# Kernel tuning notes

Hardware: AMD Instinct MI355X
Metric: run time of the kernel (lower is better)

## Reference

```python
import jax, jax.numpy as jnp
import numpy as np

D_MODEL, D_STATE, EXPAND = 1024, 32, 2
D_INNER = D_MODEL * EXPAND
B, L = 2, 2048


def setup_inputs() -> dict:
    key = jax.random.key(0)
    ks = jax.random.split(key, 10)
    s = 0.02
    return {
        "x": jax.random.normal(ks[0], (B, L, D_MODEL), dtype=jnp.float32),
        "W_in": jax.random.normal(ks[1], (D_INNER * 2, D_MODEL), dtype=jnp.float32) * s,
        "conv_w": jax.random.normal(ks[2], (D_INNER, 1, 3), dtype=jnp.float32) * 0.3,
        "conv_b": jax.random.normal(ks[3], (D_INNER,), dtype=jnp.float32) * 0.01,
        "A_log": jax.random.normal(ks[4], (D_INNER, D_STATE), dtype=jnp.float32),
        "D_skip": jnp.ones((D_INNER,), dtype=jnp.float32),
        "W_xproj": jax.random.normal(ks[5], (D_STATE * 2 + 1, D_INNER), dtype=jnp.float32) * s,
        "W_dt": jax.random.normal(ks[6], (D_INNER, 1), dtype=jnp.float32) * s,
        "b_dt": jax.random.normal(ks[7], (D_INNER,), dtype=jnp.float32) * 0.01,
        "alpha": jnp.asarray(0.5, dtype=jnp.float32),
        "W_out": jax.random.normal(ks[8], (D_MODEL, D_INNER), dtype=jnp.float32) * s,
    }


def _silu(v):
    return v * jax.nn.sigmoid(v)


def _forward(x, W_in, conv_w, conv_b, A_log, D_skip, W_xproj, W_dt, b_dt, alpha, W_out):
    # in_proj: (B, L, 2*d_inner) -> split into x_in, z
    xz = x @ W_in.T
    x_in, z = jnp.split(xz, 2, axis=-1)

    # depthwise conv1d, kernel 3, padding 1 (same-length, non-causal, as in source)
    xc = jax.lax.conv_general_dilated(
        x_in.transpose(0, 2, 1), conv_w, window_strides=(1,), padding=[(1, 1)],
        dimension_numbers=("NCH", "OIH", "NCH"), feature_group_count=D_INNER,
    ) + conv_b[None, :, None]
    x_conv = _silu(xc.transpose(0, 2, 1))  # (B, L, d_inner)

    # x_proj -> dt_raw (1), B_ssm (N), C_ssm (N)
    proj = x_conv @ W_xproj.T
    dt_raw = proj[..., :1]
    B_ssm = proj[..., 1:1 + D_STATE]
    C_ssm = proj[..., 1 + D_STATE:]
    dt = jax.nn.softplus(dt_raw @ W_dt.T + b_dt)  # (B, L, d_inner)

    A_real = -jnp.exp(A_log)           # (d_inner, d_state)
    a = jax.nn.sigmoid(alpha)

    def step(h, inp):
        dt_t, B_t, C_t, u_t = inp      # (B,d_inner), (B,N), (B,N), (B,d_inner)
        dtA = A_real[None] * dt_t[:, :, None]               # (B, d_inner, N)
        A_d = a * jnp.exp(dtA) + (1.0 - a) / (1.0 - 0.5 * dtA + 1e-6)
        h = A_d * h + (dt_t * u_t)[:, :, None] * B_t[:, None, :]
        y_t = jnp.einsum("bn,bdn->bd", C_t, h) + D_skip * u_t
        return h, y_t

    h0 = jnp.zeros((x.shape[0], D_INNER, D_STATE), dtype=x.dtype)
    xs = (dt.transpose(1, 0, 2), B_ssm.transpose(1, 0, 2),
          C_ssm.transpose(1, 0, 2), x_conv.transpose(1, 0, 2))
    _, ys = jax.lax.scan(step, h0, xs)   # (L, B, d_inner)
    y = ys.transpose(1, 0, 2) * _silu(z)
    return y @ W_out.T


def reference(x, W_in, conv_w, conv_b, A_log, D_skip, W_xproj, W_dt, b_dt, alpha, W_out):
    return _forward(x, W_in, conv_w, conv_b, A_log, D_skip, W_xproj, W_dt, b_dt, alpha, W_out)
```

## Files before the change

kernel.cpp:

```cpp
#include <hip/hip_runtime.h>

#define DM   1024
#define DI   2048
#define DST  32
#define NB   2
#define LSEQ 2048
#define BL   (NB*LSEQ)
#define LC   64
#define NC   32

using bf16   = __bf16;
using bf16x4 = __attribute__((ext_vector_type(4))) __bf16;
using bf16x8 = __attribute__((ext_vector_type(8))) __bf16;
using f32x4  = __attribute__((ext_vector_type(4))) float;
using f16x2  = __attribute__((ext_vector_type(2))) _Float16;

static __device__ __forceinline__ float sigmoidf_(float x) {
  return 1.f / (1.f + __expf(-x));
}

static __device__ __forceinline__ f16x2 pack_f16x2(float a, float b) {
  return __builtin_bit_cast(f16x2, __builtin_amdgcn_cvt_pkrtz(a, b));
}

static __device__ __forceinline__ float exp2_(float x) {
#if __has_builtin(__builtin_amdgcn_exp2f)
  return __builtin_amdgcn_exp2f(x);
#else
  return exp2f(x);
#endif
}

__global__ __launch_bounds__(256) void cast_bf16_kernel(
    const float* __restrict__ in, bf16* __restrict__ out, int n4) {
  int i = blockIdx.x * 256 + threadIdx.x;
  if (i >= n4) return;
  f32x4 v = ((const f32x4*)in)[i];
  bf16x4 o;
  #pragma unroll
  for (int j = 0; j < 4; ++j) o[j] = (bf16)v[j];
  ((bf16x4*)out)[i] = o;
}

__global__ __launch_bounds__(256) void padcast_wxp_kernel(
    const float* __restrict__ in, bf16* __restrict__ out) {
  int i = blockIdx.x * 256 + threadIdx.x;
  int k4 = i & 511;
  int r  = i >> 9;
  int src = (r < 64) ? (r + 1) : ((r == 127) ? 0 : -1);
  f32x4 v = {0.f, 0.f, 0.f, 0.f};
  if (src >= 0) v = *(const f32x4*)(in + (size_t)src * 2048 + k4 * 4);
  bf16x4 o;
  #pragma unroll
  for (int j = 0; j < 4; ++j) o[j] = (bf16)v[j];
  ((bf16x4*)out)[i] = o;
}

__global__ __launch_bounds__(256) void gemm_bt(
    const bf16* __restrict__ A, const bf16* __restrict__ B,
    float* __restrict__ C, int M, int N, int K) {
  __shared__ bf16 As[128][40];
  __shared__ bf16 Bs[128][40];

  int tid  = threadIdx.x;
  int bm   = blockIdx.y, bn = blockIdx.x;
  int row0 = bm * 128, col0 = bn * 128;
  int w    = tid >> 6, lane = tid & 63;
  int wr   = w >> 1, wc = w & 1;
  int lr   = lane & 15, lk = lane >> 4;

  f32x4 acc[4][4];
  #pragma unroll
  for (int i = 0; i < 4; ++i)
    #pragma unroll
    for (int j = 0; j < 4; ++j) acc[i][j] = f32x4{0.f, 0.f, 0.f, 0.f};

  int srow = tid >> 1;
  int scol = (tid & 1) * 16;
  const bf16* Ag = A + (size_t)(row0 + srow) * K + scol;
  const bf16* Bg = B + (size_t)(col0 + srow) * K + scol;

  for (int k0 = 0; k0 < K; k0 += 32) {
    *(bf16x8*)&As[srow][scol]     = *(const bf16x8*)(Ag + k0);
    *(bf16x8*)&As[srow][scol + 8] = *(const bf16x8*)(Ag + k0 + 8);
    *(bf16x8*)&Bs[srow][scol]     = *(const bf16x8*)(Bg + k0);
    *(bf16x8*)&Bs[srow][scol + 8] = *(const bf16x8*)(Bg + k0 + 8);
    __syncthreads();

    bf16x8 af[4], bff[4];
    #pragma unroll
    for (int mi = 0; mi < 4; ++mi)
      af[mi] = *(const bf16x8*)&As[wr * 64 + mi * 16 + lr][lk * 8];
    #pragma unroll
    for (int ni = 0; ni < 4; ++ni)
      bff[ni] = *(const bf16x8*)&Bs[wc * 64 + ni * 16 + lr][lk * 8];

    #pragma unroll
    for (int mi = 0; mi < 4; ++mi)
      #pragma unroll
      for (int ni = 0; ni < 4; ++ni)
        acc[mi][ni] = __builtin_amdgcn_mfma_f32_16x16x32_bf16(
            af[mi], bff[ni], acc[mi][ni], 0, 0, 0);
    __syncthreads();
  }

  #pragma unroll
  for (int mi = 0; mi < 4; ++mi)
    #pragma unroll
    for (int ni = 0; ni < 4; ++ni) {
      int r0 = row0 + wr * 64 + mi * 16 + lk * 4;
      int c  = col0 + wc * 64 + ni * 16 + lr;
      #pragma unroll
      for (int r = 0; r < 4; ++r)
        C[(size_t)(r0 + r) * N + c] = acc[mi][ni][r];
    }
}

__global__ __launch_bounds__(256) void conv_silu_kernel(
    const float* __restrict__ xz, bf16* __restrict__ xconv,
    const float* __restrict__ conv_w, const float* __restrict__ conv_b) {
  int i = blockIdx.x * 256 + threadIdx.x;
  int d4 = i & 511;
  int d  = d4 * 4;
  int bl = i >> 9;
  int l  = bl & (LSEQ - 1);

  const float* base = xz + (size_t)bl * (2 * DI) + d;
  f32x4 zero = {0.f, 0.f, 0.f, 0.f};
  f32x4 xm = (l > 0)        ? *(const f32x4*)(base - 2 * DI) : zero;
  f32x4 xc = *(const f32x4*)(base);
  f32x4 xp = (l < LSEQ - 1) ? *(const f32x4*)(base + 2 * DI) : zero;

  bf16x4 o;
  #pragma unroll
  for (int j = 0; j < 4; ++j) {
    float w0 = conv_w[(d + j) * 3 + 0];
    float w1 = conv_w[(d + j) * 3 + 1];
    float w2 = conv_w[(d + j) * 3 + 2];
    float v = fmaf(w0, xm[j], fmaf(w1, xc[j], fmaf(w2, xp[j], conv_b[d + j])));
    v = v * sigmoidf_(v);
    o[j] = (bf16)v;
  }
  *(bf16x4*)(xconv + (size_t)bl * DI + d) = o;
}

__global__ __launch_bounds__(256) void dtprep_kernel(
    const float* __restrict__ proj, const bf16* __restrict__ xconv,
    const float* __restrict__ W_dt, const float* __restrict__ b_dt,
    unsigned int* __restrict__ dtp) {
  int i = blockIdx.x * 256 + threadIdx.x;
  int d4 = (i & 511) * 4;
  int bl = i >> 9;
  float dtraw = proj[(size_t)bl * 128 + 127];
  f32x4 wd = *(const f32x4*)(W_dt + d4);
  f32x4 bd = *(const f32x4*)(b_dt + d4);
  bf16x4 uu = *(const bf16x4*)(xconv + (size_t)bl * DI + d4);
  uint4 o;
  #pragma unroll
  for (int j = 0; j < 4; ++j) {
    float s  = fmaf(dtraw, wd[j], bd[j]);
    float dt = (s > 15.f) ? s : __logf(1.f + __expf(s));
    float dtu = dt * (float)uu[j];
    f16x2 pk = pack_f16x2(dt, dtu);
    ((unsigned int*)&o)[j] = __builtin_bit_cast(unsigned int, pk);
  }
  *(uint4*)(dtp + (size_t)bl * 4096 + d4) = o;
}


__global__ __launch_bounds__(256, 2) void scan_phase1(
    const float* __restrict__ proj, const unsigned int* __restrict__ dtp,
    const float* __restrict__ A_log, const float* __restrict__ alpha,
    float* __restrict__ Pbuf, float* __restrict__ Hbuf) {
  int wid = threadIdx.x >> 6, lane = threadIdx.x & 63;
  int d = blockIdx.x * 256 + wid * 64 + lane;
  int b = blockIdx.y, c = blockIdx.z;

  float aG = sigmoidf_(alpha[0]), omA = 1.f - aG;

  float Ar2[DST];
  #pragma unroll
  for (int n = 0; n < DST; n += 4) {
    f32x4 al = *(const f32x4*)(A_log + (size_t)d * DST + n);
    #pragma unroll
    for (int j = 0; j < 4; ++j) Ar2[n + j] = -__expf(al[j]) * 1.44269504f;
  }

  const float* pb = proj + ((size_t)b * LSEQ + c * LC) * 128;
  const unsigned int* dc = dtp + ((size_t)b * LSEQ + c * LC) * 4096 + d;

  float h[DST], P[DST];
  #pragma unroll
  for (int n = 0; n < DST; ++n) { h[n] = 0.f; P[n] = 1.f; }

  #pragma unroll 2
  for (int t = 0; t < LC; ++t) {
    f16x2 dw = __builtin_bit_cast(f16x2, dc[(size_t)t * 4096]);
    float dt = (float)dw[0], dtu = (float)dw[1];
    const float* pr = pb + (size_t)t * 128;
    #pragma unroll
    for (int n4 = 0; n4 < 8; ++n4) {
      f32x4 Bq = *(const f32x4*)(pr + n4 * 4);
      #pragma unroll
      for (int j = 0; j < 4; ++j) {
        int n = n4 * 4 + j;
        float t1  = dt * Ar2[n];
        float ex  = exp2_(t1);
        float den = fmaf(t1, -0.34657359f, 1.000001f);
        float Ad  = fmaf(aG, ex, omA * __builtin_amdgcn_rcpf(den));
        P[n] *= Ad;
        h[n] = fmaf(Ad, h[n], dtu * Bq[j]);
      }
    }
  }
  size_t ob = (((size_t)c * NB + b) * DI + d) * DST;
  #pragma unroll
  for (int n = 0; n < DST; n += 4) {
    f32x4 pv = {P[n], P[n + 1], P[n + 2], P[n + 3]};
    f32x4 hv = {h[n], h[n + 1], h[n + 2], h[n + 3]};
    *(f32x4*)(Pbuf + ob + n) = pv;
    *(f32x4*)(Hbuf + ob + n) = hv;
  }
}

__global__ __launch_bounds__(256) void scan_phase2(
    const float* __restrict__ Pbuf, float* __restrict__ Hbuf) {
  int i = blockIdx.x * 256 + threadIdx.x;
  float H = 0.f;
  #pragma unroll
  for (int c = 0; c < NC; ++c) {
    size_t idx = (size_t)c * (NB * DI * DST) + i;
    float P  = Pbuf[idx];
    float hl = Hbuf[idx];
    Hbuf[idx] = H;
    H = fmaf(P, H, hl);
  }
}

__global__ __launch_bounds__(256, 2) void scan_phase3(
    const float* __restrict__ proj, const unsigned int* __restrict__ dtp,
    const float* __restrict__ xzf,
    const bf16* __restrict__ xconv,
    const float* __restrict__ A_log, const float* __restrict__ D_skip,
    const float* __restrict__ alpha, const float* __restrict__ Hbuf,
    bf16* __restrict__ yb) {
  int wid = threadIdx.x >> 6, lane = threadIdx.x & 63;
  int d = blockIdx.x * 256 + wid * 64 + lane;
  int b = blockIdx.y, c = blockIdx.z;

  float aG = sigmoidf_(alpha[0]), omA = 1.f - aG;
  float Dsk = D_skip[d];

  float Ar2[DST];
  #pragma unroll
  for (int n = 0; n < DST; n += 4) {
    f32x4 al = *(const f32x4*)(A_log + (size_t)d * DST + n);
    #pragma unroll
    for (int j = 0; j < 4; ++j) Ar2[n + j] = -__expf(al[j]) * 1.44269504f;
  }

  float h[DST];
  size_t ob = (((size_t)c * NB + b) * DI + d) * DST;
  #pragma unroll
  for (int n = 0; n < DST; n += 4) {
    f32x4 hv = *(const f32x4*)(Hbuf + ob + n);
    #pragma unroll
    for (int j = 0; j < 4; ++j) h[n + j] = hv[j];
  }

  const float* pb = proj + ((size_t)b * LSEQ + c * LC) * 128;
  const unsigned int* dc = dtp + ((size_t)b * LSEQ + c * LC) * 4096 + d;
  const bf16*  uc = xconv + ((size_t)b * LSEQ + c * LC) * DI + d;
  const float* zc = xzf + ((size_t)b * LSEQ + c * LC) * 4096 + 2048 + d;
  bf16*        yc = yb  + ((size_t)b * LSEQ + c * LC) * DI + d;

  #pragma unroll 2
  for (int t = 0; t < LC; ++t) {
    f16x2 dw = __builtin_bit_cast(f16x2, dc[(size_t)t * 4096]);
    float dt = (float)dw[0], dtu = (float)dw[1];
    const float* pr = pb + (size_t)t * 128;
    float p0 = 0.f, p1 = 0.f, p2 = 0.f, p3 = 0.f;
    #pragma unroll
    for (int n4 = 0; n4 < 8; ++n4) {
      f32x4 Bq = *(const f32x4*)(pr + n4 * 4);
      f32x4 Cq = *(const f32x4*)(pr + 32 + n4 * 4);
      #pragma unroll
      for (int j = 0; j < 4; ++j) {
        int n = n4 * 4 + j;
        float t1  = dt * Ar2[n];
        float ex  = exp2_(t1);
        float den = fmaf(t1, -0.34657359f, 1.000001f);
        float Ad  = fmaf(aG, ex, omA * __builtin_amdgcn_rcpf(den));
        h[n] = fmaf(Ad, h[n], dtu * Bq[j]);
        if (j == 0)      p0 = fmaf(Cq[j], h[n], p0);
        else if (j == 1) p1 = fmaf(Cq[j], h[n], p1);
        else if (j == 2) p2 = fmaf(Cq[j], h[n], p2);
        else             p3 = fmaf(Cq[j], h[n], p3);
      }
    }
    float part = (p0 + p1) + (p2 + p3);
    float u = (float)uc[(size_t)t * DI];
    float z = zc[(size_t)t * 4096];
    float y = fmaf(Dsk, u, part);
    y *= z * sigmoidf_(z);
    yc[(size_t)t * DI] = (bf16)y;
  }
}

extern "C" void kernel_launch(void* const* d_in, const int* in_sizes, int n_in,
                              void* d_out, int out_size, void* d_ws, size_t ws_size,
                              hipStream_t stream) {
  const float* x      = (const float*)d_in[0];
  const float* W_in   = (const float*)d_in[1];
  const float* conv_w = (const float*)d_in[2];
  const float* conv_b = (const float*)d_in[3];
  const float* A_log  = (const float*)d_in[4];
  const float* D_skip = (const float*)d_in[5];
  const float* W_xprj = (const float*)d_in[6];
  const float* W_dt   = (const float*)d_in[7];
  const float* b_dt   = (const float*)d_in[8];
  const float* alpha  = (const float*)d_in[9];
  const float* W_out  = (const float*)d_in[10];

  char* ws = (char*)d_ws;
  float* xz    = (float*)(ws + 0);
  bf16*  xconv = (bf16*) (ws + 67108864);
  float* proj  = (float*)(ws + 83886080);
  float* Pbuf  = (float*)(ws + 85983232);
  bf16*  yb    = (bf16*) (ws + 102760448);
  bf16*  xb    = (bf16*) (ws + 119537664);
  bf16*  winb  = (bf16*) (ws + 127926272);
  float* Hbuf  = (float*)(ws + 119537664);
  bf16*  woutb = (bf16*) (ws + 136314880);
  bf16*  wxpb  = (bf16*) (ws + 140509184);
  unsigned int* dtp = (unsigned int*)xz;

  float* out = (float*)d_out;

  cast_bf16_kernel<<<4096, 256, 0, stream>>>(x, xb, BL * DM / 4);
  cast_bf16_kernel<<<4096, 256, 0, stream>>>(W_in, winb, 2 * DI * DM / 4);
  cast_bf16_kernel<<<2048, 256, 0, stream>>>(W_out, woutb, DM * DI / 4);
  padcast_wxp_kernel<<<256, 256, 0, stream>>>(W_xprj, wxpb);

  gemm_bt<<<dim3(32, 32), 256, 0, stream>>>(xb, winb, xz, BL, 2 * DI, DM);

  conv_silu_kernel<<<8192, 256, 0, stream>>>(xz, xconv, conv_w, conv_b);

  gemm_bt<<<dim3(1, 32), 256, 0, stream>>>(xconv, wxpb, proj, BL, 128, DI);

  dtprep_kernel<<<8192, 256, 0, stream>>>(proj, xconv, W_dt, b_dt, dtp);

  scan_phase1<<<dim3(DI / 256, NB, NC), 256, 0, stream>>>(proj, dtp, A_log,
                                                          alpha, Pbuf, Hbuf);
  scan_phase2<<<512, 256, 0, stream>>>(Pbuf, Hbuf);
  scan_phase3<<<dim3(DI / 256, NB, NC), 256, 0, stream>>>(proj, dtp, xz, xconv,
                                                          A_log, D_skip, alpha,
                                                          Hbuf, yb);

  gemm_bt<<<dim3(8, 32), 256, 0, stream>>>(yb, woutb, out, BL, DM, DI);
}
```

Baseline: 394.9 us.

## Use direct global-to-LDS loads, split-K x_proj GEMM, and pack scan carries in fp16

The GEMM now stages tiles with global_load_lds instead of register round-trips, using a k-slice-major LDS layout. The narrow x_proj GEMM is split along K into 8 partial products that a separate kernel sums, which raises the block count from 32. The scan uses 64 chunks of 32 steps, packs each chunk's P and h as an fp16 pair into one word, writes the running H back in place, and raises occupancy hints to 4. This reduces scan-buffer traffic and raises parallelism, but adds a reduce kernel and fp16 precision loss in the chunk carries.

```diff
diff --git a/kernel.cpp b/kernel.cpp
--- a/kernel.cpp
+++ b/kernel.cpp
@@ -6,14 +6,17 @@
 #define NB   2
 #define LSEQ 2048
 #define BL   (NB*LSEQ)
-#define LC   64
-#define NC   32
+#define LC   32
+#define NC   64
 
 using bf16   = __bf16;
 using bf16x4 = __attribute__((ext_vector_type(4))) __bf16;
 using bf16x8 = __attribute__((ext_vector_type(8))) __bf16;
 using f32x4  = __attribute__((ext_vector_type(4))) float;
 using f16x2  = __attribute__((ext_vector_type(2))) _Float16;
+
+#define AS1(p) ((const __attribute__((address_space(1))) void*)(p))
+#define AS3(p) ((__attribute__((address_space(3))) void*)(p))
 
 static __device__ __forceinline__ float sigmoidf_(float x) {
   return 1.f / (1.f + __expf(-x));
@@ -56,11 +59,11 @@
   ((bf16x4*)out)[i] = o;
 }
 
-__global__ __launch_bounds__(256) void gemm_bt(
+__global__ __launch_bounds__(256) void gemm_lds(
     const bf16* __restrict__ A, const bf16* __restrict__ B,
-    float* __restrict__ C, int M, int N, int K) {
-  __shared__ bf16 As[128][40];
-  __shared__ bf16 Bs[128][40];
+    float* __restrict__ C, int M, int N, int K, int nz) {
+  __shared__ bf16 As2[4][128][8];
+  __shared__ bf16 Bs2[4][128][8];
 
   int tid  = threadIdx.x;
   int bm   = blockIdx.y, bn = blockIdx.x;
@@ -69,31 +72,42 @@
   int wr   = w >> 1, wc = w & 1;
   int lr   = lane & 15, lk = lane >> 4;
 
+  int seg = K / nz;
+  int kb  = blockIdx.z * seg, ke = kb + seg;
+  float* Cz = C + (size_t)blockIdx.z * ((size_t)M * N);
+
   f32x4 acc[4][4];
   #pragma unroll
   for (int i = 0; i < 4; ++i)
     #pragma unroll
     for (int j = 0; j < 4; ++j) acc[i][j] = f32x4{0.f, 0.f, 0.f, 0.f};
 
-  int srow = tid >> 1;
-  int scol = (tid & 1) * 16;
-  const bf16* Ag = A + (size_t)(row0 + srow) * K + scol;
-  const bf16* Bg = B + (size_t)(col0 + srow) * K + scol;
-
-  for (int k0 = 0; k0 < K; k0 += 32) {
-    *(bf16x8*)&As[srow][scol]     = *(const bf16x8*)(Ag + k0);
-    *(bf16x8*)&As[srow][scol + 8] = *(const bf16x8*)(Ag + k0 + 8);
-    *(bf16x8*)&Bs[srow][scol]     = *(const bf16x8*)(Bg + k0);
-    *(bf16x8*)&Bs[srow][scol + 8] = *(const bf16x8*)(Bg + k0 + 8);
+  int j0 = w * 64 + lane, j1 = 256 + w * 64 + lane;
+  int ks0 = j0 >> 7, r0s = j0 & 127;
+  int ks1 = j1 >> 7, r1s = j1 & 127;
+  const bf16* Ag0 = A + (size_t)(row0 + r0s) * K + ks0 * 8;
+  const bf16* Ag1 = A + (size_t)(row0 + r1s) * K + ks1 * 8;
+  const bf16* Bg0 = B + (size_t)(col0 + r0s) * K + ks0 * 8;
+  const bf16* Bg1 = B + (size_t)(col0 + r1s) * K + ks1 * 8;
+  bf16* AsL = &As2[0][0][0];
+  bf16* BsL = &Bs2[0][0][0];
+  int base0 = (w * 64) * 8;
+  int base1 = (256 + w * 64) * 8;
+
+  for (int k0 = kb; k0 < ke; k0 += 32) {
+    __builtin_amdgcn_global_load_lds(AS1(Ag0 + k0), AS3(AsL + base0), 16, 0, 0);
+    __builtin_amdgcn_global_load_lds(AS1(Ag1 + k0), AS3(AsL + base1), 16, 0, 0);
+    __builtin_amdgcn_global_load_lds(AS1(Bg0 + k0), AS3(BsL + base0), 16, 0, 0);
+    __builtin_amdgcn_global_load_lds(AS1(Bg1 + k0), AS3(BsL + base1), 16, 0, 0);
     __syncthreads();
 
     bf16x8 af[4], bff[4];
     #pragma unroll
     for (int mi = 0; mi < 4; ++mi)
-      af[mi] = *(const bf16x8*)&As[wr * 64 + mi * 16 + lr][lk * 8];
+      af[mi] = *(const bf16x8*)&As2[lk][wr * 64 + mi * 16 + lr][0];
     #pragma unroll
     for (int ni = 0; ni < 4; ++ni)
-      bff[ni] = *(const bf16x8*)&Bs[wc * 64 + ni * 16 + lr][lk * 8];
+      bff[ni] = *(const bf16x8*)&Bs2[lk][wc * 64 + ni * 16 + lr][0];
 
     #pragma unroll
     for (int mi = 0; mi < 4; ++mi)
@@ -112,8 +126,17 @@
       int c  = col0 + wc * 64 + ni * 16 + lr;
       #pragma unroll
       for (int r = 0; r < 4; ++r)
-        C[(size_t)(r0 + r) * N + c] = acc[mi][ni][r];
+        Cz[(size_t)(r0 + r) * N + c] = acc[mi][ni][r];
     }
+}
+
+__global__ __launch_bounds__(256) void reduce_proj_kernel(
+    const float* __restrict__ part, float* __restrict__ proj) {
+  int i = blockIdx.x * 256 + threadIdx.x;
+  f32x4 s = ((const f32x4*)part)[i];
+  #pragma unroll
+  for (int z = 1; z < 8; ++z) s += ((const f32x4*)part)[(size_t)z * 131072 + i];
+  ((f32x4*)proj)[i] = s;
 }
 
 __global__ __launch_bounds__(256) void conv_silu_kernel(
@@ -168,10 +191,10 @@
 }
 
 
-__global__ __launch_bounds__(256, 2) void scan_phase1(
+__global__ __launch_bounds__(256, 4) void scan_phase1(
     const float* __restrict__ proj, const unsigned int* __restrict__ dtp,
     const float* __restrict__ A_log, const float* __restrict__ alpha,
-    float* __restrict__ Pbuf, float* __restrict__ Hbuf) {
+    unsigned int* __restrict__ PH) {
   int wid = threadIdx.x >> 6, lane = threadIdx.x & 63;
   int d = blockIdx.x * 256 + wid * 64 + lane;
   int b = blockIdx.y, c = blockIdx.z;
@@ -215,34 +238,36 @@
   }
   size_t ob = (((size_t)c * NB + b) * DI + d) * DST;
   #pragma unroll
-  for (int n = 0; n < DST; n += 4) {
-    f32x4 pv = {P[n], P[n + 1], P[n + 2], P[n + 3]};
-    f32x4 hv = {h[n], h[n + 1], h[n + 2], h[n + 3]};
-    *(f32x4*)(Pbuf + ob + n) = pv;
-    *(f32x4*)(Hbuf + ob + n) = hv;
-  }
-}
-
-__global__ __launch_bounds__(256) void scan_phase2(
-    const float* __restrict__ Pbuf, float* __restrict__ Hbuf) {
+  for (int n4 = 0; n4 < 8; ++n4) {
+    uint4 o;
+    #pragma unroll
+    for (int j = 0; j < 4; ++j) {
+      int n = n4 * 4 + j;
+      ((unsigned int*)&o)[j] =
+          __builtin_bit_cast(unsigned int, pack_f16x2(P[n], h[n]));
+    }
+    *(uint4*)(PH + ob + n4 * 4) = o;
+  }
+}
+
+__global__ __launch_bounds__(256) void scan_phase2(unsigned int* __restrict__ PH) {
   int i = blockIdx.x * 256 + threadIdx.x;
   float H = 0.f;
-  #pragma unroll
+  #pragma unroll 4
   for (int c = 0; c < NC; ++c) {
     size_t idx = (size_t)c * (NB * DI * DST) + i;
-    float P  = Pbuf[idx];
-    float hl = Hbuf[idx];
-    Hbuf[idx] = H;
-    H = fmaf(P, H, hl);
-  }
-}
-
-__global__ __launch_bounds__(256, 2) void scan_phase3(
+    f16x2 ph = __builtin_bit_cast(f16x2, PH[idx]);
+    ((float*)PH)[idx] = H;
+    H = fmaf((float)ph[0], H, (float)ph[1]);
+  }
+}
+
+__global__ __launch_bounds__(256, 4) void scan_phase3(
     const float* __restrict__ proj, const unsigned int* __restrict__ dtp,
     const float* __restrict__ xzf,
     const bf16* __restrict__ xconv,
     const float* __restrict__ A_log, const float* __restrict__ D_skip,
-    const float* __restrict__ alpha, const float* __restrict__ Hbuf,
+    const float* __restrict__ alpha, const float* __restrict__ PH,
     bf16* __restrict__ yb) {
   int wid = threadIdx.x >> 6, lane = threadIdx.x & 63;
   int d = blockIdx.x * 256 + wid * 64 + lane;
@@ -263,7 +288,7 @@
   size_t ob = (((size_t)c * NB + b) * DI + d) * DST;
   #pragma unroll
   for (int n = 0; n < DST; n += 4) {
-    f32x4 hv = *(const f32x4*)(Hbuf + ob + n);
+    f32x4 hv = *(const f32x4*)(PH + ob + n);
     #pragma unroll
     for (int j = 0; j < 4; ++j) h[n + j] = hv[j];
   }
@@ -326,13 +351,13 @@
   float* xz    = (float*)(ws + 0);
   bf16*  xconv = (bf16*) (ws + 67108864);
   float* proj  = (float*)(ws + 83886080);
-  float* Pbuf  = (float*)(ws + 85983232);
-  bf16*  yb    = (bf16*) (ws + 102760448);
-  bf16*  xb    = (bf16*) (ws + 119537664);
-  bf16*  winb  = (bf16*) (ws + 127926272);
-  float* Hbuf  = (float*)(ws + 119537664);
-  bf16*  woutb = (bf16*) (ws + 136314880);
-  bf16*  wxpb  = (bf16*) (ws + 140509184);
+  bf16*  woutb = (bf16*) (ws + 85983232);
+  bf16*  wxpb  = (bf16*) (ws + 90177536);
+  bf16*  yb    = (bf16*) (ws + 90701824);
+  unsigned int* PH = (unsigned int*)(ws + 107479040);
+  bf16*  xb    = (bf16*) (ws + 107479040);
+  bf16*  winb  = (bf16*) (ws + 115867648);
+  float* projp = (float*)(ws + 107479040);
   unsigned int* dtp = (unsigned int*)xz;
 
   float* out = (float*)d_out;
@@ -342,20 +367,21 @@
   cast_bf16_kernel<<<2048, 256, 0, stream>>>(W_out, woutb, DM * DI / 4);
   padcast_wxp_kernel<<<256, 256, 0, stream>>>(W_xprj, wxpb);
 
-  gemm_bt<<<dim3(32, 32), 256, 0, stream>>>(xb, winb, xz, BL, 2 * DI, DM);
+  gemm_lds<<<dim3(32, 32, 1), 256, 0, stream>>>(xb, winb, xz, BL, 2 * DI, DM, 1);
 
   conv_silu_kernel<<<8192, 256, 0, stream>>>(xz, xconv, conv_w, conv_b);
 
-  gemm_bt<<<dim3(1, 32), 256, 0, stream>>>(xconv, wxpb, proj, BL, 128, DI);
+  gemm_lds<<<dim3(1, 32, 8), 256, 0, stream>>>(xconv, wxpb, projp, BL, 128, DI, 8);
+  reduce_proj_kernel<<<512, 256, 0, stream>>>(projp, proj);
 
   dtprep_kernel<<<8192, 256, 0, stream>>>(proj, xconv, W_dt, b_dt, dtp);
 
   scan_phase1<<<dim3(DI / 256, NB, NC), 256, 0, stream>>>(proj, dtp, A_log,
-                                                          alpha, Pbuf, Hbuf);
-  scan_phase2<<<512, 256, 0, stream>>>(Pbuf, Hbuf);
+                                                          alpha, PH);
+  scan_phase2<<<512, 256, 0, stream>>>(PH);
   scan_phase3<<<dim3(DI / 256, NB, NC), 256, 0, stream>>>(proj, dtp, xz, xconv,
                                                           A_log, D_skip, alpha,
-                                                          Hbuf, yb);
-
-  gemm_bt<<<dim3(8, 32), 256, 0, stream>>>(yb, woutb, out, BL, DM, DI);
-}
+                                                          (const float*)PH, yb);
+
+  gemm_lds<<<dim3(8, 32, 1), 256, 0, stream>>>(yb, woutb, out, BL, DM, DI, 1);
+}
```

Result: slower. 406.3 us (+2.9%).
